# Kernel tuning notes

Measured on AMD Instinct MI355X. Metric: run time of the kernel, lower is better.

## Reference

```python
import jax, jax.numpy as jnp
import numpy as np

N, E = 100000, 500000
IN_CH, OUT_CH, MSG_DIM, TIME_DIM, HEADS = 128, 128, 128, 128, 2
C = OUT_CH // HEADS  # per-head channels
EDGE_DIM = MSG_DIM + TIME_DIM


def setup_inputs() -> dict:
    key = jax.random.key(0)
    ks = jax.random.split(key, 16)
    inp = {
        "x": jax.random.normal(ks[0], (N, IN_CH), jnp.float32),
        "last_update": jax.random.uniform(ks[1], (N,), jnp.float32) * 1000.0,
        "t": jax.random.uniform(ks[2], (E,), jnp.float32) * 1000.0,
        "msg": jax.random.normal(ks[3], (E, MSG_DIM), jnp.float32),
        "edge_index": jax.random.randint(ks[4], (2, E), 0, N, jnp.int64),
        # TimeEncoder: Linear(1, TIME_DIM) then cos
        "time_w": jax.random.normal(ks[5], (TIME_DIM,), jnp.float32) / jnp.sqrt(1.0),
        "time_b": jax.random.normal(ks[6], (TIME_DIM,), jnp.float32) * 0.02,
        # TransformerConv linears (stored [in, out] for x @ W)
        "Wq": jax.random.normal(ks[7], (IN_CH, HEADS * C), jnp.float32) / np.sqrt(IN_CH),
        "bq": jnp.zeros((HEADS * C,), jnp.float32),
        "Wk": jax.random.normal(ks[8], (IN_CH, HEADS * C), jnp.float32) / np.sqrt(IN_CH),
        "bk": jnp.zeros((HEADS * C,), jnp.float32),
        "Wv": jax.random.normal(ks[9], (IN_CH, HEADS * C), jnp.float32) / np.sqrt(IN_CH),
        "bv": jnp.zeros((HEADS * C,), jnp.float32),
        "We": jax.random.normal(ks[10], (EDGE_DIM, HEADS * C), jnp.float32) / np.sqrt(EDGE_DIM),  # lin_edge, no bias
        "Wskip": jax.random.normal(ks[11], (IN_CH, HEADS * C), jnp.float32) / np.sqrt(IN_CH),
        "bskip": jnp.zeros((HEADS * C,), jnp.float32),
    }
    return inp


def reference(x, last_update, t, msg, edge_index, time_w, time_b,
              Wq, bq, Wk, bk, Wv, bv, We, Wskip, bskip):
    src = edge_index[0]
    dst = edge_index[1]

    # relative time encoding: cos(Linear(1 -> TIME_DIM))
    rel_t = t - last_update[src]                              # [E]
    rel_t_enc = jnp.cos(rel_t[:, None] * time_w[None, :] + time_b[None, :])  # [E, T]
    edge_attr = jnp.concatenate([rel_t_enc, msg], axis=-1)    # [E, EDGE_DIM]

    # project nodes, then gather per-edge (query at dst, key/value at src)
    q = (x @ Wq + bq).reshape(N, HEADS, C)[dst]               # [E, H, C]
    k = (x @ Wk + bk).reshape(N, HEADS, C)[src]
    v = (x @ Wv + bv).reshape(N, HEADS, C)[src]
    e = (edge_attr @ We).reshape(E, HEADS, C)                 # [E, H, C]

    k = k + e
    alpha = jnp.sum(q * k, axis=-1) / jnp.sqrt(jnp.float32(C))  # [E, H]

    # segment softmax over edges sharing the same destination node
    m = jax.ops.segment_max(alpha, dst, num_segments=N)       # [N, H]
    alpha = jnp.exp(alpha - m[dst])
    s = jax.ops.segment_sum(alpha, dst, num_segments=N)       # [N, H]
    alpha = alpha / (s[dst] + 1e-16)

    # weighted value (value also receives edge projection), scatter-add to dst
    out_e = (v + e) * alpha[..., None]                        # [E, H, C]
    out = jax.ops.segment_sum(out_e, dst, num_segments=N)     # [N, H, C]
    out = out.reshape(N, HEADS * C)

    # root/skip connection
    out = out + x @ Wskip + bskip
    return out
```

## Files before the change

### kernel.cpp

```cpp
#include <hip/hip_runtime.h>
#include <hip/hip_bf16.h>

#define NN 100000
#define EE 500000

typedef __attribute__((ext_vector_type(8))) short short8v;
typedef __attribute__((ext_vector_type(4))) float f32x4;

__device__ __forceinline__ short f2bf(float f) {
  unsigned u = __builtin_bit_cast(unsigned, f);
  u += 0x7fffu + ((u >> 16) & 1u);
  return (short)(u >> 16);
}

__device__ __forceinline__ void barlds() {
  asm volatile("s_waitcnt lgkmcnt(0)" ::: "memory");
  __builtin_amdgcn_s_barrier();
  asm volatile("" ::: "memory");
}

__global__ __launch_bounds__(256) void k_prep(
    const float* __restrict__ Wq, const float* __restrict__ Wk,
    const float* __restrict__ Wv, const float* __restrict__ Wsk,
    const float* __restrict__ We, const float* __restrict__ tw,
    const float* __restrict__ tb,
    short* __restrict__ Btfrag, short* __restrict__ Wefrag,
    float* __restrict__ twp, float* __restrict__ tbp)
{
  int idx = blockIdx.x * 256 + threadIdx.x;
  if (idx < 65536) {
    int b = idx & 7, lane = (idx >> 3) & 63, kt = (idx >> 9) & 3, tn = (idx >> 11) & 7, cb = idx >> 14;
    int k = kt * 32 + (lane >> 4) * 8 + b;
    int c = tn * 16 + (lane & 15);
    const float* W = cb == 0 ? Wq : cb == 1 ? Wk : cb == 2 ? Wv : Wsk;
    Btfrag[idx] = f2bf(W[k * 128 + c]);
  } else if (idx < 98304) {
    int i2 = idx - 65536;
    int b = i2 & 7, lane = (i2 >> 3) & 63, kt = (i2 >> 9) & 7, strip = i2 >> 12;
    int k = kt * 32 + (lane >> 4) * 8 + b;
    int c = strip * 16 + (lane & 15);
    Wefrag[i2] = f2bf(We[k * 128 + c]);
  } else if (idx < 100352) {
    int i3 = idx - 98304;
    int which = i3 >> 10;
    int r = (i3 >> 7) & 7;
    int c = i3 & 127;
    int lc = ((c >> 3) ^ r) * 8 + (c & 7);
    if (which) tbp[r * 128 + c] = tb[lc];
    else       twp[r * 128 + c] = tw[lc];
  }
}

__global__ __launch_bounds__(256) void k_xcast(const float* __restrict__ x,
                                               unsigned short* __restrict__ xb)
{
  size_t base = ((size_t)blockIdx.x * 256 + threadIdx.x) * 8;
  f32x4 a = *(const f32x4*)(x + base);
  f32x4 b = *(const f32x4*)(x + base + 4);
  short8v w;
  #pragma unroll
  for (int j = 0; j < 4; ++j) { w[j] = f2bf(a[j]); w[4 + j] = f2bf(b[j]); }
  *(short8v*)(xb + base) = w;
}

__global__ __launch_bounds__(256) void k_zero(int* __restrict__ p, int n)
{
  int i = blockIdx.x * 256 + threadIdx.x;
  if (i < n) p[i] = 0;
}

__global__ __launch_bounds__(256) void k_hist(const int* __restrict__ ei, int* __restrict__ cnt)
{
  int e = blockIdx.x * 256 + threadIdx.x;
  if (e < EE) atomicAdd(&cnt[ei[EE + e]], 1);
}

__global__ __launch_bounds__(256) void k_scan_a(const int* __restrict__ cnt,
    int* __restrict__ offtmp, int* __restrict__ bsum)
{
  __shared__ int sc[256];
  int t = threadIdx.x;
  int i = blockIdx.x * 256 + t;
  int v = (i < NN) ? cnt[i] : 0;
  sc[t] = v;
  __syncthreads();
  for (int d = 1; d < 256; d <<= 1) {
    int add = (t >= d) ? sc[t - d] : 0;
    __syncthreads();
    sc[t] += add;
    __syncthreads();
  }
  if (i < NN) offtmp[i] = sc[t] - v;
  if (t == 255) bsum[blockIdx.x] = sc[255];
}

__global__ __launch_bounds__(512) void k_scan_b(const int* __restrict__ bsum,
                                                int* __restrict__ bbase)
{
  __shared__ int sc[512];
  int t = threadIdx.x;
  int v = (t < 391) ? bsum[t] : 0;
  sc[t] = v;
  __syncthreads();
  for (int d = 1; d < 512; d <<= 1) {
    int add = (t >= d) ? sc[t - d] : 0;
    __syncthreads();
    sc[t] += add;
    __syncthreads();
  }
  bbase[t] = sc[t] - v;
}

__global__ __launch_bounds__(256) void k_scatter(const int* __restrict__ ei,
    const int* __restrict__ offtmp, const int* __restrict__ bbase,
    int* __restrict__ cur, int* __restrict__ sorted)
{
  int e = blockIdx.x * 256 + threadIdx.x;
  if (e < EE) {
    int d = ei[EE + e];
    int pos = offtmp[d] + bbase[d >> 8] + atomicAdd(&cur[d], 1);
    sorted[pos] = e;
  }
}

__global__ __launch_bounds__(256) void k_emeta(const int* __restrict__ ei,
    const float* __restrict__ tt, const float* __restrict__ lu,
    const int* __restrict__ sorted, int4* __restrict__ emeta)
{
  int i = blockIdx.x * 256 + threadIdx.x;
  if (i < EE) {
    int eid = sorted[i];
    int sv = ei[eid];
    int4 m;
    m.x = eid; m.y = sv; m.z = ei[EE + eid];
    m.w = __float_as_int(tt[eid] - lu[sv]);
    emeta[i] = m;
  }
}

__global__ __launch_bounds__(512) void k_mperm(const float* __restrict__ msg,
    const int* __restrict__ sorted, unsigned short* __restrict__ msgp)
{
  int t = blockIdx.x * 512 + threadIdx.x;
  int i = t >> 4;
  int c = t & 15;
  if (i < EE) {
    int eid = sorted[i];
    const float* mp = msg + (size_t)eid * 128 + c * 8;
    f32x4 m0 = *(const f32x4*)mp, m1 = *(const f32x4*)(mp + 4);
    short8v w;
    #pragma unroll
    for (int j = 0; j < 4; ++j) { w[j] = f2bf(m0[j]); w[4 + j] = f2bf(m1[j]); }
    *(short8v*)(msgp + (size_t)i * 128 + c * 8) = w;
  }
}

__global__ __launch_bounds__(512) void k_main(
    const unsigned short* __restrict__ xb, const float* __restrict__ msg,
    const unsigned short* __restrict__ msgp, const int use_mp,
    const float* __restrict__ twp, const float* __restrict__ tbp,
    const short* __restrict__ Btfrag, const short* __restrict__ Wefrag,
    const float* __restrict__ bq, const float* __restrict__ bk,
    const float* __restrict__ bv, const float* __restrict__ bsk,
    const int* __restrict__ offtmp, const int* __restrict__ bbase,
    const int4* __restrict__ emeta, float* __restrict__ out)
{
  __shared__ short XS[64 * 128];
  __shared__ short EAT[64 * 256];
  __shared__ short QL[64 * 128];
  __shared__ short KL[64 * 128];
  __shared__ short VT[128 * 64];
  __shared__ short PLm[64 * 64];
  __shared__ short PLm2[64 * 64];
  __shared__ float sdenL[128];
  __shared__ int dslot[64];

  const int tid = threadIdx.x;
  const int nb0 = blockIdx.x * 64;
  const int wid = tid >> 6, lane = tid & 63;
  const int g = lane >> 4, lr = lane & 15, l7 = lr & 7;
  const int el = tid >> 3, p = tid & 7;
  const int er7 = el & 7;
  const int plg = p ^ er7;
  const int cme = wid * 16 + lr;
  const int cmeh = cme >> 3, cml = cme & 7;

  const float bqc = bq[cme], bkc = bk[cme], bvc = bv[cme], bskc = bsk[cme];
  const short8v ONEB = {16256,16256,16256,16256,16256,16256,16256,16256};

  {
    int node = nb0 + el;
    short8v a = {0,0,0,0,0,0,0,0}, b = a;
    if (node < NN) {
      const unsigned short* xp = xb + (size_t)node * 128;
      a = *(const short8v*)(xp + plg * 8);
      b = *(const short8v*)(xp + plg * 8 + 64);
    }
    *(short8v*)&XS[el * 128 + p * 8] = a;
    *(short8v*)&XS[el * 128 + p * 8 + 64] = b;
  }
  barlds();
  {
    f32x4 qacc[4], skacc[4];
    #pragma unroll
    for (int eg = 0; eg < 4; ++eg) {
      qacc[eg] = (f32x4){0.f, 0.f, 0.f, 0.f};
      skacc[eg] = qacc[eg];
    }
    #pragma unroll
    for (int kt = 0; kt < 4; ++kt) {
      short8v bqf = *(const short8v*)(Btfrag + (size_t)(((0 + wid) * 4 + kt) * 64 + lane) * 8);
      short8v bsf = *(const short8v*)(Btfrag + (size_t)(((24 + wid) * 4 + kt) * 64 + lane) * 8);
      const int sw = (((kt << 2) | g) ^ l7) << 3;
      #pragma unroll
      for (int eg = 0; eg < 4; ++eg) {
        const short8v a = *(const short8v*)&XS[(eg * 16 + lr) * 128 + sw];
        qacc[eg] = __builtin_amdgcn_mfma_f32_16x16x32_bf16(a, bqf, qacc[eg], 0, 0, 0);
        skacc[eg] = __builtin_amdgcn_mfma_f32_16x16x32_bf16(a, bsf, skacc[eg], 0, 0, 0);
      }
    }
    #pragma unroll
    for (int eg = 0; eg < 4; ++eg)
      #pragma unroll
      for (int rg = 0; rg < 4; ++rg) {
        int row = eg * 16 + g * 4 + rg;
        int node = nb0 + row;
        QL[row * 128 + ((cmeh ^ (row & 7)) << 3) + cml] = f2bf(qacc[eg][rg] + bqc);
        if (node < NN) out[(size_t)node * 128 + cme] = skacc[eg][rg] + bskc;
      }
  }

  const int beg = offtmp[nb0] + bbase[nb0 >> 8];
  const int end = (nb0 + 64 < NN) ? (offtmp[nb0 + 64] + bbase[(nb0 + 64) >> 8]) : EE;

  f32x4 acc[4], sdacc;
  #pragma unroll
  for (int rtt = 0; rtt < 4; ++rtt) acc[rtt] = (f32x4){0.f, 0.f, 0.f, 0.f};
  sdacc = (f32x4){0.f, 0.f, 0.f, 0.f};

  int pdst = 0; float prelt = 0.f; bool pval = false;
  short8v px0 = {0,0,0,0,0,0,0,0}, px1 = px0, pmb0 = px0, pmb1 = px0;
  {
    int i = beg + el;
    pval = i < end;
    if (pval) {
      int4 m = emeta[i];
      pdst = m.z; prelt = __int_as_float(m.w);
      const unsigned short* xp = xb + (size_t)m.y * 128 + plg * 8;
      px0 = *(const short8v*)xp;
      px1 = *(const short8v*)(xp + 64);
      if (use_mp) {
        const unsigned short* mp = msgp + (size_t)i * 128 + plg * 8;
        pmb0 = *(const short8v*)mp;
        pmb1 = *(const short8v*)(mp + 64);
      } else {
        const float* mp = msg + (size_t)m.x * 128 + plg * 8;
        f32x4 m0 = *(const f32x4*)mp,        m1 = *(const f32x4*)(mp + 4);
        f32x4 m2 = *(const f32x4*)(mp + 64), m3 = *(const f32x4*)(mp + 68);
        #pragma unroll
        for (int j = 0; j < 4; ++j) {
          pmb0[j] = f2bf(m0[j]); pmb0[4 + j] = f2bf(m1[j]);
          pmb1[j] = f2bf(m2[j]); pmb1[4 + j] = f2bf(m3[j]);
        }
      }
    }
  }
  barlds();

  for (int t0 = beg; t0 < end; t0 += 64) {
    if (p == 0) dslot[el] = pval ? (pdst - nb0) : -1;
    *(short8v*)&XS[el * 128 + p * 8] = px0;
    *(short8v*)&XS[el * 128 + p * 8 + 64] = px1;
    *(short8v*)&EAT[el * 256 + 128 + p * 8] = pmb0;
    *(short8v*)&EAT[el * 256 + 128 + p * 8 + 64] = pmb1;
    {
      const float* twr = twp + er7 * 128;
      const float* tbr = tbp + er7 * 128;
      f32x4 w0 = *(const f32x4*)(twr + p * 8),      w1 = *(const f32x4*)(twr + p * 8 + 4);
      f32x4 b0 = *(const f32x4*)(tbr + p * 8),      b1 = *(const f32x4*)(tbr + p * 8 + 4);
      f32x4 w2 = *(const f32x4*)(twr + p * 8 + 64), w3 = *(const f32x4*)(twr + p * 8 + 68);
      f32x4 b2 = *(const f32x4*)(tbr + p * 8 + 64), b3 = *(const f32x4*)(tbr + p * 8 + 68);
      short8v ta, tb2;
      #pragma unroll
      for (int j = 0; j < 4; ++j) {
        ta[j]      = f2bf(__cosf(fmaf(prelt, w0[j], b0[j])));
        ta[4 + j]  = f2bf(__cosf(fmaf(prelt, w1[j], b1[j])));
        tb2[j]     = f2bf(__cosf(fmaf(prelt, w2[j], b2[j])));
        tb2[4 + j] = f2bf(__cosf(fmaf(prelt, w3[j], b3[j])));
      }
      *(short8v*)&EAT[el * 256 + p * 8] = ta;
      *(short8v*)&EAT[el * 256 + p * 8 + 64] = tb2;
    }
    barlds();

    {
      int i = t0 + 64 + el;
      pval = i < end;
      if (pval) {
        int4 m = emeta[i];
        pdst = m.z; prelt = __int_as_float(m.w);
        const unsigned short* xp = xb + (size_t)m.y * 128 + plg * 8;
        px0 = *(const short8v*)xp;
        px1 = *(const short8v*)(xp + 64);
        if (use_mp) {
          const unsigned short* mp = msgp + (size_t)i * 128 + plg * 8;
          pmb0 = *(const short8v*)mp;
          pmb1 = *(const short8v*)(mp + 64);
        } else {
          const float* mp = msg + (size_t)m.x * 128 + plg * 8;
          f32x4 m0 = *(const f32x4*)mp,        m1 = *(const f32x4*)(mp + 4);
          f32x4 m2 = *(const f32x4*)(mp + 64), m3 = *(const f32x4*)(mp + 68);
          #pragma unroll
          for (int j = 0; j < 4; ++j) {
            pmb0[j] = f2bf(m0[j]); pmb0[4 + j] = f2bf(m1[j]);
            pmb1[j] = f2bf(m2[j]); pmb1[4 + j] = f2bf(m3[j]);
          }
        }
      }
    }

    f32x4 ae[4];
    ae[0] = (f32x4){0.f, 0.f, 0.f, 0.f}; ae[1] = ae[0]; ae[2] = ae[0]; ae[3] = ae[0];
    #pragma unroll
    for (int kt = 0; kt < 8; ++kt) {
      short8v wef = *(const short8v*)(Wefrag + (size_t)((wid * 8 + kt) * 64 + lane) * 8);
      const int sw = (((kt << 2) | g) ^ l7) << 3;
      #pragma unroll
      for (int eg = 0; eg < 4; ++eg) {
        const short8v a = *(const short8v*)&EAT[(eg * 16 + lr) * 256 + sw];
        ae[eg] = __builtin_amdgcn_mfma_f32_16x16x32_bf16(a, wef, ae[eg], 0, 0, 0);
      }
    }
    f32x4 ak[4], av[4];
    ak[0] = (f32x4){0.f, 0.f, 0.f, 0.f}; ak[1] = ak[0]; ak[2] = ak[0]; ak[3] = ak[0];
    av[0] = ak[0]; av[1] = ak[0]; av[2] = ak[0]; av[3] = ak[0];
    #pragma unroll
    for (int kt = 0; kt < 4; ++kt) {
      short8v wkf = *(const short8v*)(Btfrag + (size_t)(((8 + wid) * 4 + kt) * 64 + lane) * 8);
      short8v wvf = *(const short8v*)(Btfrag + (size_t)(((16 + wid) * 4 + kt) * 64 + lane) * 8);
      const int sw = (((kt << 2) | g) ^ l7) << 3;
      #pragma unroll
      for (int eg = 0; eg < 4; ++eg) {
        const short8v a = *(const short8v*)&XS[(eg * 16 + lr) * 128 + sw];
        ak[eg] = __builtin_amdgcn_mfma_f32_16x16x32_bf16(a, wkf, ak[eg], 0, 0, 0);
        av[eg] = __builtin_amdgcn_mfma_f32_16x16x32_bf16(a, wvf, av[eg], 0, 0, 0);
      }
    }
    #pragma unroll
    for (int eg = 0; eg < 4; ++eg)
      #pragma unroll
      for (int rg = 0; rg < 4; ++rg) {
        int e = eg * 16 + g * 4 + rg;
        float kh = ak[eg][rg] + bkc + ae[eg][rg];
        float vh = av[eg][rg] + bvc + ae[eg][rg];
        KL[e * 128 + ((cmeh ^ (e & 7)) << 3) + cml] = f2bf(kh);
        VT[cme * 64 + ((((e >> 3) ^ cml)) << 3) + (e & 7)] = f2bf(vh);
      }
    barlds();

    {
      const int rt = wid >> 1, ct0 = (wid & 1) * 2;
      short8v qa[4];
      #pragma unroll
      for (int kt = 0; kt < 4; ++kt)
        qa[kt] = *(const short8v*)&QL[(rt * 16 + lr) * 128 + ((((kt << 2) | g) ^ l7) << 3)];
      #pragma unroll
      for (int c2 = 0; c2 < 2; ++c2) {
        const int ct = ct0 + c2;
        f32x4 s0 = (f32x4){0.f, 0.f, 0.f, 0.f};
        f32x4 s1 = (f32x4){0.f, 0.f, 0.f, 0.f};
        #pragma unroll
        for (int kt = 0; kt < 4; ++kt) {
          const short8v kbf = *(const short8v*)&KL[(ct * 16 + lr) * 128 + ((((kt << 2) | g) ^ l7) << 3)];
          if (kt < 2) s0 = __builtin_amdgcn_mfma_f32_16x16x32_bf16(qa[kt], kbf, s0, 0, 0, 0);
          else        s1 = __builtin_amdgcn_mfma_f32_16x16x32_bf16(qa[kt], kbf, s1, 0, 0, 0);
        }
        const int col = ct * 16 + lr;
        const int dsc = dslot[col];
        #pragma unroll
        for (int rg = 0; rg < 4; ++rg) {
          int row = rt * 16 + g * 4 + rg;
          bool hit = (dsc == row);
          float pv0 = hit ? __expf(s0[rg] * 0.125f) : 0.f;
          float pv1 = hit ? __expf(s1[rg] * 0.125f) : 0.f;
          int off = row * 64 + ((((col >> 3) ^ (row & 7))) << 3) + (col & 7);
          PLm[off] = f2bf(pv0);
          PLm2[off] = f2bf(pv1);
        }
      }
    }
    barlds();

    {
      const short* PH = (wid < 4) ? PLm : PLm2;
      const int rt4 = wid & 3;
      const short8v vb0 = *(const short8v*)&VT[cme * 64 + ((g ^ cml) << 3)];
      const short8v vb1 = *(const short8v*)&VT[cme * 64 + (((4 | g) ^ cml) << 3)];
      #pragma unroll
      for (int rtt = 0; rtt < 4; ++rtt) {
        const short8v pa0 = *(const short8v*)&PH[(rtt * 16 + lr) * 64 + ((g ^ l7) << 3)];
        const short8v pa1 = *(const short8v*)&PH[(rtt * 16 + lr) * 64 + (((4 | g) ^ l7) << 3)];
        acc[rtt] = __builtin_amdgcn_mfma_f32_16x16x32_bf16(pa0, vb0, acc[rtt], 0, 0, 0);
        acc[rtt] = __builtin_amdgcn_mfma_f32_16x16x32_bf16(pa1, vb1, acc[rtt], 0, 0, 0);
        if (rt4 == rtt) {
          sdacc = __builtin_amdgcn_mfma_f32_16x16x32_bf16(pa0, ONEB, sdacc, 0, 0, 0);
          sdacc = __builtin_amdgcn_mfma_f32_16x16x32_bf16(pa1, ONEB, sdacc, 0, 0, 0);
        }
      }
    }
  }

  if (lr == 0) {
    #pragma unroll
    for (int rg = 0; rg < 4; ++rg)
      sdenL[(wid >> 2) * 64 + (wid & 3) * 16 + g * 4 + rg] = sdacc[rg];
  }
  barlds();
  #pragma unroll
  for (int rtt = 0; rtt < 4; ++rtt)
    #pragma unroll
    for (int rg = 0; rg < 4; ++rg) {
      int row = rtt * 16 + g * 4 + rg;
      int node = nb0 + row;
      if (node < NN) {
        float den = sdenL[(wid >> 2) * 64 + row] + 1e-16f;
        size_t o = (size_t)node * 128 + cme;
        out[o] = out[o] + acc[rtt][rg] / den;
      }
    }
}

extern "C" void kernel_launch(void* const* d_in, const int* in_sizes, int n_in,
                              void* d_out, int out_size, void* d_ws, size_t ws_size,
                              hipStream_t stream) {
  const float* x    = (const float*)d_in[0];
  const float* lu   = (const float*)d_in[1];
  const float* tt   = (const float*)d_in[2];
  const float* msg  = (const float*)d_in[3];
  const int*   ei   = (const int*)d_in[4];
  const float* timew = (const float*)d_in[5];
  const float* timeb = (const float*)d_in[6];
  const float* Wq   = (const float*)d_in[7];
  const float* bq   = (const float*)d_in[8];
  const float* Wk   = (const float*)d_in[9];
  const float* bk   = (const float*)d_in[10];
  const float* Wv   = (const float*)d_in[11];
  const float* bv   = (const float*)d_in[12];
  const float* We   = (const float*)d_in[13];
  const float* Wsk  = (const float*)d_in[14];
  const float* bsk  = (const float*)d_in[15];
  float* out = (float*)d_out;

  char* wsp = (char*)d_ws;
  unsigned short* xbw  = (unsigned short*)wsp;
  short* Btfrag = (short*)(wsp + 51200000);
  short* Wefrag = (short*)(wsp + 51331072);
  float* twp    = (float*)(wsp + 51396608);
  float* tbp    = (float*)(wsp + 51400704);
  int* cnt      = (int*)(wsp + 51404800);
  int* cur      = (int*)(wsp + 51804800);
  int* offtmp   = (int*)(wsp + 52204800);
  int* bsum     = (int*)(wsp + 52605184);
  int* bbase    = (int*)(wsp + 52607232);
  int* sorted   = (int*)(wsp + 52609280);
  int4* emeta   = (int4*)(wsp + 54609280);
  unsigned short* msgp = (unsigned short*)(wsp + 62609280);
  const int use_mp = (ws_size >= (size_t)190609280) ? 1 : 0;

  k_zero<<<782, 256, 0, stream>>>(cnt, 200000);
  k_prep<<<392, 256, 0, stream>>>(Wq, Wk, Wv, Wsk, We, timew, timeb,
                                  Btfrag, Wefrag, twp, tbp);
  k_xcast<<<6250, 256, 0, stream>>>(x, xbw);
  k_hist<<<1954, 256, 0, stream>>>(ei, cnt);
  k_scan_a<<<391, 256, 0, stream>>>(cnt, offtmp, bsum);
  k_scan_b<<<1, 512, 0, stream>>>(bsum, bbase);
  k_scatter<<<1954, 256, 0, stream>>>(ei, offtmp, bbase, cur, sorted);
  k_emeta<<<1954, 256, 0, stream>>>(ei, tt, lu, sorted, emeta);
  if (use_mp) k_mperm<<<15625, 512, 0, stream>>>(msg, sorted, msgp);
  k_main<<<1563, 512, 0, stream>>>(xbw, msg, msgp, use_mp, twp, tbp,
                                   Btfrag, Wefrag, bq, bk, bv, bsk,
                                   offtmp, bbase, emeta, out);
}
```

Baseline: 468.0 us.

## Alias k_main shared-memory buffers and raise occupancy with launch bounds

Merges XS/EAT and KL/VT/PLm/PLm2 into one aliased LDS region, which cuts shared memory per block. Adds two barriers so the aliased regions are not overwritten while still in use. Requests 4 waves per EU through launch_bounds so more blocks can share a CU. Moves the XOR swizzle from the global-load address to the LDS store address, which removes the pre-swizzled time-weight tables and their prep work. The extra barriers and tighter register budget could cost some per-block throughput.

```diff
diff --git a/kernel.cpp b/kernel.cpp
--- a/kernel.cpp
+++ b/kernel.cpp
@@ -22,10 +22,8 @@
 __global__ __launch_bounds__(256) void k_prep(
     const float* __restrict__ Wq, const float* __restrict__ Wk,
     const float* __restrict__ Wv, const float* __restrict__ Wsk,
-    const float* __restrict__ We, const float* __restrict__ tw,
-    const float* __restrict__ tb,
-    short* __restrict__ Btfrag, short* __restrict__ Wefrag,
-    float* __restrict__ twp, float* __restrict__ tbp)
+    const float* __restrict__ We,
+    short* __restrict__ Btfrag, short* __restrict__ Wefrag)
 {
   int idx = blockIdx.x * 256 + threadIdx.x;
   if (idx < 65536) {
@@ -40,14 +38,6 @@
     int k = kt * 32 + (lane >> 4) * 8 + b;
     int c = strip * 16 + (lane & 15);
     Wefrag[i2] = f2bf(We[k * 128 + c]);
-  } else if (idx < 100352) {
-    int i3 = idx - 98304;
-    int which = i3 >> 10;
-    int r = (i3 >> 7) & 7;
-    int c = i3 & 127;
-    int lc = ((c >> 3) ^ r) * 8 + (c & 7);
-    if (which) tbp[r * 128 + c] = tb[lc];
-    else       twp[r * 128 + c] = tw[lc];
   }
 }
 
@@ -155,25 +145,27 @@
   }
 }
 
-__global__ __launch_bounds__(512) void k_main(
+__global__ __launch_bounds__(512, 4) void k_main(
     const unsigned short* __restrict__ xb, const float* __restrict__ msg,
     const unsigned short* __restrict__ msgp, const int use_mp,
-    const float* __restrict__ twp, const float* __restrict__ tbp,
+    const float* __restrict__ tw, const float* __restrict__ tb,
     const short* __restrict__ Btfrag, const short* __restrict__ Wefrag,
     const float* __restrict__ bq, const float* __restrict__ bk,
     const float* __restrict__ bv, const float* __restrict__ bsk,
     const int* __restrict__ offtmp, const int* __restrict__ bbase,
     const int4* __restrict__ emeta, float* __restrict__ out)
 {
-  __shared__ short XS[64 * 128];
-  __shared__ short EAT[64 * 256];
+  __shared__ short R[24576];
   __shared__ short QL[64 * 128];
-  __shared__ short KL[64 * 128];
-  __shared__ short VT[128 * 64];
-  __shared__ short PLm[64 * 64];
-  __shared__ short PLm2[64 * 64];
   __shared__ float sdenL[128];
   __shared__ int dslot[64];
+
+  short* const XS = R;
+  short* const EAT = R + 8192;
+  short* const KL = R;
+  short* const VT = R + 8192;
+  short* const PLm = R + 16384;
+  short* const PLm2 = R + 20480;
 
   const int tid = threadIdx.x;
   const int nb0 = blockIdx.x * 64;
@@ -181,7 +173,7 @@
   const int g = lane >> 4, lr = lane & 15, l7 = lr & 7;
   const int el = tid >> 3, p = tid & 7;
   const int er7 = el & 7;
-  const int plg = p ^ er7;
+  const int psw = p ^ er7;
   const int cme = wid * 16 + lr;
   const int cmeh = cme >> 3, cml = cme & 7;
 
@@ -192,12 +184,12 @@
     int node = nb0 + el;
     short8v a = {0,0,0,0,0,0,0,0}, b = a;
     if (node < NN) {
-      const unsigned short* xp = xb + (size_t)node * 128;
-      a = *(const short8v*)(xp + plg * 8);
-      b = *(const short8v*)(xp + plg * 8 + 64);
-    }
-    *(short8v*)&XS[el * 128 + p * 8] = a;
-    *(short8v*)&XS[el * 128 + p * 8 + 64] = b;
+      const unsigned short* xp = xb + (size_t)node * 128 + p * 8;
+      a = *(const short8v*)xp;
+      b = *(const short8v*)(xp + 64);
+    }
+    *(short8v*)&XS[el * 128 + psw * 8] = a;
+    *(short8v*)&XS[el * 128 + psw * 8 + 64] = b;
   }
   barlds();
   {
@@ -246,15 +238,15 @@
     if (pval) {
       int4 m = emeta[i];
       pdst = m.z; prelt = __int_as_float(m.w);
-      const unsigned short* xp = xb + (size_t)m.y * 128 + plg * 8;
+      const unsigned short* xp = xb + (size_t)m.y * 128 + p * 8;
       px0 = *(const short8v*)xp;
       px1 = *(const short8v*)(xp + 64);
       if (use_mp) {
-        const unsigned short* mp = msgp + (size_t)i * 128 + plg * 8;
+        const unsigned short* mp = msgp + (size_t)i * 128 + p * 8;
         pmb0 = *(const short8v*)mp;
         pmb1 = *(const short8v*)(mp + 64);
       } else {
-        const float* mp = msg + (size_t)m.x * 128 + plg * 8;
+        const float* mp = msg + (size_t)m.x * 128 + p * 8;
         f32x4 m0 = *(const f32x4*)mp,        m1 = *(const f32x4*)(mp + 4);
         f32x4 m2 = *(const f32x4*)(mp + 64), m3 = *(const f32x4*)(mp + 68);
         #pragma unroll
@@ -269,17 +261,15 @@
 
   for (int t0 = beg; t0 < end; t0 += 64) {
     if (p == 0) dslot[el] = pval ? (pdst - nb0) : -1;
-    *(short8v*)&XS[el * 128 + p * 8] = px0;
-    *(short8v*)&XS[el * 128 + p * 8 + 64] = px1;
-    *(short8v*)&EAT[el * 256 + 128 + p * 8] = pmb0;
-    *(short8v*)&EAT[el * 256 + 128 + p * 8 + 64] = pmb1;
+    *(short8v*)&XS[el * 128 + psw * 8] = px0;
+    *(short8v*)&XS[el * 128 + psw * 8 + 64] = px1;
+    *(short8v*)&EAT[el * 256 + 128 + psw * 8] = pmb0;
+    *(short8v*)&EAT[el * 256 + 128 + psw * 8 + 64] = pmb1;
     {
-      const float* twr = twp + er7 * 128;
-      const float* tbr = tbp + er7 * 128;
-      f32x4 w0 = *(const f32x4*)(twr + p * 8),      w1 = *(const f32x4*)(twr + p * 8 + 4);
-      f32x4 b0 = *(const f32x4*)(tbr + p * 8),      b1 = *(const f32x4*)(tbr + p * 8 + 4);
-      f32x4 w2 = *(const f32x4*)(twr + p * 8 + 64), w3 = *(const f32x4*)(twr + p * 8 + 68);
-      f32x4 b2 = *(const f32x4*)(tbr + p * 8 + 64), b3 = *(const f32x4*)(tbr + p * 8 + 68);
+      f32x4 w0 = *(const f32x4*)(tw + p * 8),      w1 = *(const f32x4*)(tw + p * 8 + 4);
+      f32x4 b0 = *(const f32x4*)(tb + p * 8),      b1 = *(const f32x4*)(tb + p * 8 + 4);
+      f32x4 w2 = *(const f32x4*)(tw + p * 8 + 64), w3 = *(const f32x4*)(tw + p * 8 + 68);
+      f32x4 b2 = *(const f32x4*)(tb + p * 8 + 64), b3 = *(const f32x4*)(tb + p * 8 + 68);
       short8v ta, tb2;
       #pragma unroll
       for (int j = 0; j < 4; ++j) {
@@ -288,8 +278,8 @@
         tb2[j]     = f2bf(__cosf(fmaf(prelt, w2[j], b2[j])));
         tb2[4 + j] = f2bf(__cosf(fmaf(prelt, w3[j], b3[j])));
       }
-      *(short8v*)&EAT[el * 256 + p * 8] = ta;
-      *(short8v*)&EAT[el * 256 + p * 8 + 64] = tb2;
+      *(short8v*)&EAT[el * 256 + psw * 8] = ta;
+      *(short8v*)&EAT[el * 256 + psw * 8 + 64] = tb2;
     }
     barlds();
 
@@ -299,15 +289,15 @@
       if (pval) {
         int4 m = emeta[i];
         pdst = m.z; prelt = __int_as_float(m.w);
-        const unsigned short* xp = xb + (size_t)m.y * 128 + plg * 8;
+        const unsigned short* xp = xb + (size_t)m.y * 128 + p * 8;
         px0 = *(const short8v*)xp;
         px1 = *(const short8v*)(xp + 64);
         if (use_mp) {
-          const unsigned short* mp = msgp + (size_t)i * 128 + plg * 8;
+          const unsigned short* mp = msgp + (size_t)i * 128 + p * 8;
           pmb0 = *(const short8v*)mp;
           pmb1 = *(const short8v*)(mp + 64);
         } else {
-          const float* mp = msg + (size_t)m.x * 128 + plg * 8;
+          const float* mp = msg + (size_t)m.x * 128 + p * 8;
           f32x4 m0 = *(const f32x4*)mp,        m1 = *(const f32x4*)(mp + 4);
           f32x4 m2 = *(const f32x4*)(mp + 64), m3 = *(const f32x4*)(mp + 68);
           #pragma unroll
@@ -346,6 +336,8 @@
         av[eg] = __builtin_amdgcn_mfma_f32_16x16x32_bf16(a, wvf, av[eg], 0, 0, 0);
       }
     }
+    barlds();
+
     #pragma unroll
     for (int eg = 0; eg < 4; ++eg)
       #pragma unroll
@@ -408,6 +400,7 @@
         }
       }
     }
+    barlds();
   }
 
   if (lr == 0) {
@@ -455,8 +448,6 @@
   unsigned short* xbw  = (unsigned short*)wsp;
   short* Btfrag = (short*)(wsp + 51200000);
   short* Wefrag = (short*)(wsp + 51331072);
-  float* twp    = (float*)(wsp + 51396608);
-  float* tbp    = (float*)(wsp + 51400704);
   int* cnt      = (int*)(wsp + 51404800);
   int* cur      = (int*)(wsp + 51804800);
   int* offtmp   = (int*)(wsp + 52204800);
@@ -468,8 +459,7 @@
   const int use_mp = (ws_size >= (size_t)190609280) ? 1 : 0;
 
   k_zero<<<782, 256, 0, stream>>>(cnt, 200000);
-  k_prep<<<392, 256, 0, stream>>>(Wq, Wk, Wv, Wsk, We, timew, timeb,
-                                  Btfrag, Wefrag, twp, tbp);
+  k_prep<<<384, 256, 0, stream>>>(Wq, Wk, Wv, Wsk, We, Btfrag, Wefrag);
   k_xcast<<<6250, 256, 0, stream>>>(x, xbw);
   k_hist<<<1954, 256, 0, stream>>>(ei, cnt);
   k_scan_a<<<391, 256, 0, stream>>>(cnt, offtmp, bsum);
@@ -477,7 +467,7 @@
   k_scatter<<<1954, 256, 0, stream>>>(ei, offtmp, bbase, cur, sorted);
   k_emeta<<<1954, 256, 0, stream>>>(ei, tt, lu, sorted, emeta);
   if (use_mp) k_mperm<<<15625, 512, 0, stream>>>(msg, sorted, msgp);
-  k_main<<<1563, 512, 0, stream>>>(xbw, msg, msgp, use_mp, twp, tbp,
+  k_main<<<1563, 512, 0, stream>>>(xbw, msg, msgp, use_mp, timew, timeb,
                                    Btfrag, Wefrag, bq, bk, bv, bsk,
                                    offtmp, bbase, emeta, out);
 }
```

After: 836.1 us. +78.7%, slower.
